# Kernel optimization log

Hardware: AMD Instinct MI355X
Metric: run time of the kernel (lower is better)

The kernel has to match this reference:

```python
import jax, jax.numpy as jnp
import numpy as np

T, B, I, H = 2048, 64, 256, 256


def setup_inputs() -> dict:
    key = jax.random.key(0)
    k_x, k_w, k_hh = jax.random.split(key, 3)
    x = jax.random.normal(k_x, (T, B, I), dtype=jnp.float32)
    # input-to-hidden weight for the 3 gates [r, z, n], torch GRU layout [3H, I]
    W_ih = jax.random.normal(k_w, (3 * H, I), dtype=jnp.float32) * (1.0 / np.sqrt(H))
    # biases are zero-filled in IndGRU.__init__ but remain parameters
    b_ih = jnp.zeros((3 * H,), dtype=jnp.float32)
    b_hh = jnp.zeros((3 * H,), dtype=jnp.float32)
    # per-unit (diagonal) recurrent weights, uniform(-1, 1), rows = [r, z, n]
    w_hh = jax.random.uniform(k_hh, (3, H), dtype=jnp.float32, minval=-1.0, maxval=1.0)
    return {"x": x, "W_ih": W_ih, "b_ih": b_ih, "b_hh": b_hh, "w_hh": w_hh}


def reference(x, W_ih, b_ih, b_hh, w_hh):
    # x: [T, B, I] time-major (torch GRU default). Diagonal-recurrence GRU:
    # the hidden-to-hidden matmul collapses to an elementwise multiply per gate.
    Bsz = x.shape[1]
    Hsz = w_hh.shape[1]
    # Precompute all input-side gate pre-activations in one big GEMM: [T, B, 3H]
    gx = jnp.einsum('tbi,gi->tbg', x, W_ih) + b_ih
    gxr, gxz, gxn = jnp.split(gx, 3, axis=-1)
    w_hr, w_hz, w_hn = w_hh[0], w_hh[1], w_hh[2]
    b_hr, b_hz, b_hn = jnp.split(b_hh, 3)

    def step(h, g):
        xr, xz, xn = g
        r = jax.nn.sigmoid(xr + w_hr * h + b_hr)
        z = jax.nn.sigmoid(xz + w_hz * h + b_hz)
        n = jnp.tanh(xn + r * (w_hn * h + b_hn))
        h_new = (1.0 - z) * n + z * h
        return h_new, h_new

    h0 = jnp.zeros((Bsz, Hsz), dtype=x.dtype)
    h_n, out = jax.lax.scan(step, h0, (gxr, gxz, gxn))
    # torch GRU returns (output [T,B,H], h_n [num_layers=1, B, H])
    return out, h_n[None]
```

## Files before the change

kernel.cpp:

```cpp
#include <hip/hip_runtime.h>
#include <stdint.h>

#define T_LEN 2048
#define BATCH 64
#define I_DIM 256
#define H_DIM 256
#define N3    768
#define M_ROWS (T_LEN*BATCH)
#define L2E 1.4426950408889634f

typedef __attribute__((ext_vector_type(4))) float  f32x4;
typedef __attribute__((ext_vector_type(4))) unsigned short u16x4;
typedef __attribute__((ext_vector_type(4))) unsigned int   u32x4;
typedef __attribute__((ext_vector_type(8))) __bf16 bf16x8;

__device__ __forceinline__ unsigned short f2bf_rne(float f) {
    uint32_t u = __float_as_uint(f);
    u += 0x7FFFu + ((u >> 16) & 1u);
    return (unsigned short)(u >> 16);
}
__device__ __forceinline__ float bf2f(unsigned short b) {
    return __uint_as_float(((uint32_t)b) << 16);
}

__global__ void convert_w(const float* __restrict__ W,
                          unsigned short* __restrict__ Whi,
                          unsigned short* __restrict__ Wlo) {
    int idx = blockIdx.x * 256 + threadIdx.x;
    int row = idx >> 8;
    float scale = (row < 2*H_DIM) ? -L2E : -2.0f*L2E;
    float v = W[idx] * scale;
    unsigned short hi = f2bf_rne(v);
    Whi[idx] = hi;
    Wlo[idx] = f2bf_rne(v - bf2f(hi));
}

#define BM 128
#define BN 128
#define BK 64

__device__ __forceinline__ int lds_swz(int row, int kbyte) {
    return row * 128 + (kbyte ^ ((row & 7) << 4));
}

__global__ __launch_bounds__(256, 2) void gemm_gx(
        const float* __restrict__ X,
        const unsigned short* __restrict__ Whi,
        const unsigned short* __restrict__ Wlo,
        float* __restrict__ gx) {
    __shared__ unsigned short sAhi[BM*BK], sAlo[BM*BK], sBhi[BN*BK], sBlo[BN*BK];

    int wg   = blockIdx.x;
    int orig = (wg & 7) * 768 + (wg >> 3);
    int mblk = orig / 6, nblk = orig - mblk * 6;
    int m0 = mblk * BM, n0 = nblk * BN;

    int tid  = threadIdx.x;
    int lane = tid & 63, wid = tid >> 6;
    int wm = wid >> 1, wn = wid & 1;

    int acol = tid & 15, arow = tid >> 4;
    int bcol = tid & 7,  brow = tid >> 3;

    f32x4 acc[4][4] = {};

    for (int kb = 0; kb < 4; ++kb) {
        f32x4 ra[8];
        u32x4 rbh[4], rbl[4];
        #pragma unroll
        for (int p = 0; p < 8; ++p) {
            int row = p*16 + arow;
            ra[p] = *(const f32x4*)(X + (size_t)(m0+row)*I_DIM + kb*BK + acol*4);
        }
        #pragma unroll
        for (int p = 0; p < 4; ++p) {
            int row = p*32 + brow;
            rbh[p] = *(const u32x4*)(Whi + (size_t)(n0+row)*I_DIM + kb*BK + bcol*8);
            rbl[p] = *(const u32x4*)(Wlo + (size_t)(n0+row)*I_DIM + kb*BK + bcol*8);
        }
        __syncthreads();
        #pragma unroll
        for (int p = 0; p < 8; ++p) {
            int row = p*16 + arow;
            u16x4 hi, lo;
            #pragma unroll
            for (int e = 0; e < 4; ++e) {
                float v = ra[p][e];
                unsigned short hb = f2bf_rne(v);
                hi[e] = hb;
                lo[e] = f2bf_rne(v - bf2f(hb));
            }
            int off = lds_swz(row, acol*8);
            *(u16x4*)((char*)sAhi + off) = hi;
            *(u16x4*)((char*)sAlo + off) = lo;
        }
        #pragma unroll
        for (int p = 0; p < 4; ++p) {
            int row = p*32 + brow;
            int off = lds_swz(row, bcol*16);
            *(u32x4*)((char*)sBhi + off) = rbh[p];
            *(u32x4*)((char*)sBlo + off) = rbl[p];
        }
        __syncthreads();
        #pragma unroll
        for (int kk = 0; kk < 2; ++kk) {
            bf16x8 ah[4], al[4], bh[4], bl[4];
            #pragma unroll
            for (int mi = 0; mi < 4; ++mi) {
                int row = wm*64 + mi*16 + (lane & 15);
                int off = lds_swz(row, kk*64 + (lane >> 4)*16);
                ah[mi] = *(const bf16x8*)((const char*)sAhi + off);
                al[mi] = *(const bf16x8*)((const char*)sAlo + off);
            }
            #pragma unroll
            for (int ni = 0; ni < 4; ++ni) {
                int row = wn*64 + ni*16 + (lane & 15);
                int off = lds_swz(row, kk*64 + (lane >> 4)*16);
                bh[ni] = *(const bf16x8*)((const char*)sBhi + off);
                bl[ni] = *(const bf16x8*)((const char*)sBlo + off);
            }
            #pragma unroll
            for (int mi = 0; mi < 4; ++mi)
              #pragma unroll
              for (int ni = 0; ni < 4; ++ni) {
                acc[mi][ni] = __builtin_amdgcn_mfma_f32_16x16x32_bf16(ah[mi], bh[ni], acc[mi][ni], 0,0,0);
                acc[mi][ni] = __builtin_amdgcn_mfma_f32_16x16x32_bf16(ah[mi], bl[ni], acc[mi][ni], 0,0,0);
                acc[mi][ni] = __builtin_amdgcn_mfma_f32_16x16x32_bf16(al[mi], bh[ni], acc[mi][ni], 0,0,0);
              }
        }
    }
    #pragma unroll
    for (int mi = 0; mi < 4; ++mi) {
        int rbase = m0 + wm*64 + mi*16 + (lane >> 4)*4;
        #pragma unroll
        for (int ni = 0; ni < 4; ++ni) {
            int col = n0 + wn*64 + ni*16 + (lane & 15);
            #pragma unroll
            for (int j = 0; j < 4; ++j)
                gx[(size_t)(rbase + j)*N3 + col] = acc[mi][ni][j];
        }
    }
}

__global__ __launch_bounds__(64) void indgru_scan(
        const float* __restrict__ gx, const float* __restrict__ bih,
        const float* __restrict__ bhh, const float* __restrict__ whh,
        float* __restrict__ out) {
    int lane = threadIdx.x;
    int b = blockIdx.x >> 2;
    int h = (blockIdx.x & 3) * 64 + lane;

    float whr = -L2E  * whh[h];
    float whz = -L2E  * whh[H_DIM + h];
    float whn = -2.0f*L2E * whh[2*H_DIM + h];
    float cr  = -L2E  * (bih[h] + bhh[h]);
    float cz  = -L2E  * (bih[H_DIM+h] + bhh[H_DIM+h]);
    float cn  = -2.0f*L2E * bih[2*H_DIM+h];
    float bhn = -2.0f*L2E * bhh[2*H_DIM+h];

    const size_t sg = (size_t)BATCH * N3;
    const size_t so = (size_t)BATCH * H_DIM;
    const float* pr = gx + (size_t)b*N3 + h;
    float* po = out + (size_t)b*H_DIM + h;

    float fr[16], fz[16], fn[16];
    {
        const float* p = pr;
        #pragma unroll
        for (int i = 0; i < 16; ++i) {
            fr[i] = p[0]; fz[i] = p[H_DIM]; fn[i] = p[2*H_DIM];
            p += sg;
        }
    }
    const float* prp = pr + 16*sg;
    float hv = 0.f;

    for (int tb = 0; tb < T_LEN/16 - 1; ++tb) {
        #pragma unroll
        for (int j = 0; j < 16; ++j) {
            float ur = fr[j] + cr, uz = fz[j] + cz, un = fn[j] + cn;
            fr[j] = prp[0]; fz[j] = prp[H_DIM]; fn[j] = prp[2*H_DIM];
            prp += sg;
            float er = __builtin_amdgcn_exp2f(fmaf(whr, hv, ur));
            float r  = __builtin_amdgcn_rcpf(1.f + er);
            float ez = __builtin_amdgcn_exp2f(fmaf(whz, hv, uz));
            float z  = __builtin_amdgcn_rcpf(1.f + ez);
            float mn = fmaf(whn, hv, bhn);
            float en = __builtin_amdgcn_exp2f(fmaf(r, mn, un));
            float q  = __builtin_amdgcn_rcpf(1.f + en);
            float hp1 = hv + 1.f;
            hv = fmaf(z, fmaf(-2.f, q, hp1), fmaf(2.f, q, -1.f));
            *po = hv; po += so;
        }
    }
    #pragma unroll
    for (int j = 0; j < 16; ++j) {
        float ur = fr[j] + cr, uz = fz[j] + cz, un = fn[j] + cn;
        float er = __builtin_amdgcn_exp2f(fmaf(whr, hv, ur));
        float r  = __builtin_amdgcn_rcpf(1.f + er);
        float ez = __builtin_amdgcn_exp2f(fmaf(whz, hv, uz));
        float z  = __builtin_amdgcn_rcpf(1.f + ez);
        float mn = fmaf(whn, hv, bhn);
        float en = __builtin_amdgcn_exp2f(fmaf(r, mn, un));
        float q  = __builtin_amdgcn_rcpf(1.f + en);
        float hp1 = hv + 1.f;
        hv = fmaf(z, fmaf(-2.f, q, hp1), fmaf(2.f, q, -1.f));
        *po = hv; po += so;
    }
    out[(size_t)T_LEN * so + (size_t)b*H_DIM + h] = hv;
}

extern "C" void kernel_launch(void* const* d_in, const int* in_sizes, int n_in,
                              void* d_out, int out_size, void* d_ws, size_t ws_size,
                              hipStream_t stream) {
    const float* x   = (const float*)d_in[0];
    const float* Wih = (const float*)d_in[1];
    const float* bih = (const float*)d_in[2];
    const float* bhh = (const float*)d_in[3];
    const float* whh = (const float*)d_in[4];
    float* out = (float*)d_out;

    char* ws = (char*)d_ws;
    float* gxbuf = (float*)ws;
    unsigned short* Whi = (unsigned short*)(ws + (size_t)M_ROWS*N3*sizeof(float));
    unsigned short* Wlo = Whi + (size_t)N3*I_DIM;

    convert_w<<<(N3*I_DIM)/256, 256, 0, stream>>>(Wih, Whi, Wlo);
    gemm_gx<<<(M_ROWS/BM)*(N3/BN), 256, 0, stream>>>(x, Whi, Wlo, gxbuf);
    indgru_scan<<<BATCH*(H_DIM/64), 64, 0, stream>>>(gxbuf, bih, bhh, whh, out);
}
```

Baseline: 521.1 us.

## Switch GEMM to single-pass fp16 MFMA and store gate pre-activations as fp16

Replaces the three-pass bf16 hi/lo split GEMM with a single fp16 MFMA pass, which cuts matrix work and LDS traffic to about a third and raises the occupancy hint to 4. The intermediate gx buffer is now stored in fp16, halving the write and re-read traffic between the GEMM and the scan. The scan kernel gets explicit double-buffered 16-step prefetch blocks. The cost is precision: fp16 inputs and fp16 gate pre-activations lose accuracy compared with the near-fp32 split, and fp16 could overflow for large activations.

```diff
diff --git a/kernel.cpp b/kernel.cpp
--- a/kernel.cpp
+++ b/kernel.cpp
@@ -9,30 +9,18 @@
 #define M_ROWS (T_LEN*BATCH)
 #define L2E 1.4426950408889634f
 
+typedef _Float16 f16;
 typedef __attribute__((ext_vector_type(4))) float  f32x4;
-typedef __attribute__((ext_vector_type(4))) unsigned short u16x4;
 typedef __attribute__((ext_vector_type(4))) unsigned int   u32x4;
-typedef __attribute__((ext_vector_type(8))) __bf16 bf16x8;
-
-__device__ __forceinline__ unsigned short f2bf_rne(float f) {
-    uint32_t u = __float_as_uint(f);
-    u += 0x7FFFu + ((u >> 16) & 1u);
-    return (unsigned short)(u >> 16);
-}
-__device__ __forceinline__ float bf2f(unsigned short b) {
-    return __uint_as_float(((uint32_t)b) << 16);
-}
+typedef __attribute__((ext_vector_type(8))) _Float16 f16x8;
+typedef __attribute__((ext_vector_type(4))) _Float16 f16x4;
 
 __global__ void convert_w(const float* __restrict__ W,
-                          unsigned short* __restrict__ Whi,
-                          unsigned short* __restrict__ Wlo) {
+                          f16* __restrict__ Whf) {
     int idx = blockIdx.x * 256 + threadIdx.x;
     int row = idx >> 8;
     float scale = (row < 2*H_DIM) ? -L2E : -2.0f*L2E;
-    float v = W[idx] * scale;
-    unsigned short hi = f2bf_rne(v);
-    Whi[idx] = hi;
-    Wlo[idx] = f2bf_rne(v - bf2f(hi));
+    Whf[idx] = (f16)(W[idx] * scale);
 }
 
 #define BM 128
@@ -43,12 +31,11 @@
     return row * 128 + (kbyte ^ ((row & 7) << 4));
 }
 
-__global__ __launch_bounds__(256, 2) void gemm_gx(
+__global__ __launch_bounds__(256, 4) void gemm_gx(
         const float* __restrict__ X,
-        const unsigned short* __restrict__ Whi,
-        const unsigned short* __restrict__ Wlo,
-        float* __restrict__ gx) {
-    __shared__ unsigned short sAhi[BM*BK], sAlo[BM*BK], sBhi[BN*BK], sBlo[BN*BK];
+        const f16* __restrict__ Whf,
+        f16* __restrict__ gx) {
+    __shared__ f16 sA[BM*BK], sB[BN*BK];
 
     int wg   = blockIdx.x;
     int orig = (wg & 7) * 768 + (wg >> 3);
@@ -66,7 +53,7 @@
 
     for (int kb = 0; kb < 4; ++kb) {
         f32x4 ra[8];
-        u32x4 rbh[4], rbl[4];
+        u32x4 rb[4];
         #pragma unroll
         for (int p = 0; p < 8; ++p) {
             int row = p*16 + arow;
@@ -75,58 +62,41 @@
         #pragma unroll
         for (int p = 0; p < 4; ++p) {
             int row = p*32 + brow;
-            rbh[p] = *(const u32x4*)(Whi + (size_t)(n0+row)*I_DIM + kb*BK + bcol*8);
-            rbl[p] = *(const u32x4*)(Wlo + (size_t)(n0+row)*I_DIM + kb*BK + bcol*8);
+            rb[p] = *(const u32x4*)(Whf + (size_t)(n0+row)*I_DIM + kb*BK + bcol*8);
         }
         __syncthreads();
         #pragma unroll
         for (int p = 0; p < 8; ++p) {
             int row = p*16 + arow;
-            u16x4 hi, lo;
-            #pragma unroll
-            for (int e = 0; e < 4; ++e) {
-                float v = ra[p][e];
-                unsigned short hb = f2bf_rne(v);
-                hi[e] = hb;
-                lo[e] = f2bf_rne(v - bf2f(hb));
-            }
-            int off = lds_swz(row, acol*8);
-            *(u16x4*)((char*)sAhi + off) = hi;
-            *(u16x4*)((char*)sAlo + off) = lo;
+            f16x4 hv;
+            #pragma unroll
+            for (int e = 0; e < 4; ++e) hv[e] = (f16)ra[p][e];
+            *(f16x4*)((char*)sA + lds_swz(row, acol*8)) = hv;
         }
         #pragma unroll
         for (int p = 0; p < 4; ++p) {
             int row = p*32 + brow;
-            int off = lds_swz(row, bcol*16);
-            *(u32x4*)((char*)sBhi + off) = rbh[p];
-            *(u32x4*)((char*)sBlo + off) = rbl[p];
+            *(u32x4*)((char*)sB + lds_swz(row, bcol*16)) = rb[p];
         }
         __syncthreads();
         #pragma unroll
         for (int kk = 0; kk < 2; ++kk) {
-            bf16x8 ah[4], al[4], bh[4], bl[4];
+            f16x8 a[4], b[4];
             #pragma unroll
             for (int mi = 0; mi < 4; ++mi) {
                 int row = wm*64 + mi*16 + (lane & 15);
-                int off = lds_swz(row, kk*64 + (lane >> 4)*16);
-                ah[mi] = *(const bf16x8*)((const char*)sAhi + off);
-                al[mi] = *(const bf16x8*)((const char*)sAlo + off);
+                a[mi] = *(const f16x8*)((const char*)sA + lds_swz(row, kk*64 + (lane >> 4)*16));
             }
             #pragma unroll
             for (int ni = 0; ni < 4; ++ni) {
                 int row = wn*64 + ni*16 + (lane & 15);
-                int off = lds_swz(row, kk*64 + (lane >> 4)*16);
-                bh[ni] = *(const bf16x8*)((const char*)sBhi + off);
-                bl[ni] = *(const bf16x8*)((const char*)sBlo + off);
+                b[ni] = *(const f16x8*)((const char*)sB + lds_swz(row, kk*64 + (lane >> 4)*16));
             }
             #pragma unroll
             for (int mi = 0; mi < 4; ++mi)
               #pragma unroll
-              for (int ni = 0; ni < 4; ++ni) {
-                acc[mi][ni] = __builtin_amdgcn_mfma_f32_16x16x32_bf16(ah[mi], bh[ni], acc[mi][ni], 0,0,0);
-                acc[mi][ni] = __builtin_amdgcn_mfma_f32_16x16x32_bf16(ah[mi], bl[ni], acc[mi][ni], 0,0,0);
-                acc[mi][ni] = __builtin_amdgcn_mfma_f32_16x16x32_bf16(al[mi], bh[ni], acc[mi][ni], 0,0,0);
-              }
+              for (int ni = 0; ni < 4; ++ni)
+                acc[mi][ni] = __builtin_amdgcn_mfma_f32_16x16x32_f16(a[mi], b[ni], acc[mi][ni], 0,0,0);
         }
     }
     #pragma unroll
@@ -137,13 +107,13 @@
             int col = n0 + wn*64 + ni*16 + (lane & 15);
             #pragma unroll
             for (int j = 0; j < 4; ++j)
-                gx[(size_t)(rbase + j)*N3 + col] = acc[mi][ni][j];
+                gx[(size_t)(rbase + j)*N3 + col] = (f16)acc[mi][ni][j];
         }
     }
 }
 
 __global__ __launch_bounds__(64) void indgru_scan(
-        const float* __restrict__ gx, const float* __restrict__ bih,
+        const f16* __restrict__ gx, const float* __restrict__ bih,
         const float* __restrict__ bhh, const float* __restrict__ whh,
         float* __restrict__ out) {
     int lane = threadIdx.x;
@@ -160,54 +130,54 @@
 
     const size_t sg = (size_t)BATCH * N3;
     const size_t so = (size_t)BATCH * H_DIM;
-    const float* pr = gx + (size_t)b*N3 + h;
+    const f16* pr = gx + (size_t)b*N3 + h;
     float* po = out + (size_t)b*H_DIM + h;
 
-    float fr[16], fz[16], fn[16];
-    {
-        const float* p = pr;
-        #pragma unroll
-        for (int i = 0; i < 16; ++i) {
-            fr[i] = p[0]; fz[i] = p[H_DIM]; fn[i] = p[2*H_DIM];
-            p += sg;
-        }
+    f16 Ar[16], Az[16], An[16], Br[16], Bz[16], Bn[16];
+    float hv = 0.f;
+
+#define LOAD16(R, Z, N, tblk) do {                                  \
+        const f16* _p = pr + (size_t)(tblk)*16*sg;                  \
+        _Pragma("unroll")                                           \
+        for (int _i = 0; _i < 16; ++_i) {                           \
+            R[_i] = _p[0]; Z[_i] = _p[H_DIM]; N[_i] = _p[2*H_DIM];  \
+            _p += sg;                                               \
+        }                                                           \
+    } while (0)
+
+#define PROC16(R, Z, N) do {                                        \
+        _Pragma("unroll")                                           \
+        for (int _j = 0; _j < 16; ++_j) {                           \
+            float ur = (float)R[_j] + cr;                           \
+            float uz = (float)Z[_j] + cz;                           \
+            float un = (float)N[_j] + cn;                           \
+            float er = __builtin_amdgcn_exp2f(fmaf(whr, hv, ur));   \
+            float r  = __builtin_amdgcn_rcpf(1.f + er);             \
+            float ez = __builtin_amdgcn_exp2f(fmaf(whz, hv, uz));   \
+            float z  = __builtin_amdgcn_rcpf(1.f + ez);             \
+            float mn = fmaf(whn, hv, bhn);                          \
+            float en = __builtin_amdgcn_exp2f(fmaf(r, mn, un));     \
+            float q  = __builtin_amdgcn_rcpf(1.f + en);             \
+            float hp1 = hv + 1.f;                                   \
+            hv = fmaf(z, fmaf(-2.f, q, hp1), fmaf(2.f, q, -1.f));   \
+            *po = hv; po += so;                                     \
+        }                                                           \
+    } while (0)
+
+    LOAD16(Ar, Az, An, 0);
+    for (int i = 0; i < 63; ++i) {
+        LOAD16(Br, Bz, Bn, 2*i+1);
+        PROC16(Ar, Az, An);
+        LOAD16(Ar, Az, An, 2*i+2);
+        PROC16(Br, Bz, Bn);
     }
-    const float* prp = pr + 16*sg;
-    float hv = 0.f;
-
-    for (int tb = 0; tb < T_LEN/16 - 1; ++tb) {
-        #pragma unroll
-        for (int j = 0; j < 16; ++j) {
-            float ur = fr[j] + cr, uz = fz[j] + cz, un = fn[j] + cn;
-            fr[j] = prp[0]; fz[j] = prp[H_DIM]; fn[j] = prp[2*H_DIM];
-            prp += sg;
-            float er = __builtin_amdgcn_exp2f(fmaf(whr, hv, ur));
-            float r  = __builtin_amdgcn_rcpf(1.f + er);
-            float ez = __builtin_amdgcn_exp2f(fmaf(whz, hv, uz));
-            float z  = __builtin_amdgcn_rcpf(1.f + ez);
-            float mn = fmaf(whn, hv, bhn);
-            float en = __builtin_amdgcn_exp2f(fmaf(r, mn, un));
-            float q  = __builtin_amdgcn_rcpf(1.f + en);
-            float hp1 = hv + 1.f;
-            hv = fmaf(z, fmaf(-2.f, q, hp1), fmaf(2.f, q, -1.f));
-            *po = hv; po += so;
-        }
-    }
-    #pragma unroll
-    for (int j = 0; j < 16; ++j) {
-        float ur = fr[j] + cr, uz = fz[j] + cz, un = fn[j] + cn;
-        float er = __builtin_amdgcn_exp2f(fmaf(whr, hv, ur));
-        float r  = __builtin_amdgcn_rcpf(1.f + er);
-        float ez = __builtin_amdgcn_exp2f(fmaf(whz, hv, uz));
-        float z  = __builtin_amdgcn_rcpf(1.f + ez);
-        float mn = fmaf(whn, hv, bhn);
-        float en = __builtin_amdgcn_exp2f(fmaf(r, mn, un));
-        float q  = __builtin_amdgcn_rcpf(1.f + en);
-        float hp1 = hv + 1.f;
-        hv = fmaf(z, fmaf(-2.f, q, hp1), fmaf(2.f, q, -1.f));
-        *po = hv; po += so;
-    }
+    LOAD16(Br, Bz, Bn, 127);
+    PROC16(Ar, Az, An);
+    PROC16(Br, Bz, Bn);
+
     out[(size_t)T_LEN * so + (size_t)b*H_DIM + h] = hv;
+#undef LOAD16
+#undef PROC16
 }
 
 extern "C" void kernel_launch(void* const* d_in, const int* in_sizes, int n_in,
@@ -221,11 +191,10 @@
     float* out = (float*)d_out;
 
     char* ws = (char*)d_ws;
-    float* gxbuf = (float*)ws;
-    unsigned short* Whi = (unsigned short*)(ws + (size_t)M_ROWS*N3*sizeof(float));
-    unsigned short* Wlo = Whi + (size_t)N3*I_DIM;
-
-    convert_w<<<(N3*I_DIM)/256, 256, 0, stream>>>(Wih, Whi, Wlo);
-    gemm_gx<<<(M_ROWS/BM)*(N3/BN), 256, 0, stream>>>(x, Whi, Wlo, gxbuf);
+    f16* gxbuf = (f16*)ws;
+    f16* Whf = (f16*)(ws + (size_t)M_ROWS*N3*sizeof(f16));
+
+    convert_w<<<(N3*I_DIM)/256, 256, 0, stream>>>(Wih, Whf);
+    gemm_gx<<<(M_ROWS/BM)*(N3/BN), 256, 0, stream>>>(x, Whf, gxbuf);
     indgru_scan<<<BATCH*(H_DIM/64), 64, 0, stream>>>(gxbuf, bih, bhh, whh, out);
 }
```

Result: slower. 583.6 us (+12.0%).
